# Optimization experiments

Measured on AMD Instinct MI355X. Metric: run time of the kernel, lower is better.

The kernel has to match this reference:

```python
import jax, jax.numpy as jnp
import numpy as np

# Static config (matches init_kwargs); spatial shapes must be static for jit.
SPATIAL = [(96, 96), (48, 48), (24, 24), (12, 12)]  # (H_l, W_l)
D, NH, NL, NP = 256, 8, 4, 4
DH = D // NH
DFFN = 1024


def _ln(x, g, b):
    m = jnp.mean(x, -1, keepdims=True)
    v = jnp.var(x, -1, keepdims=True)
    return (x - m) * jax.lax.rsqrt(v + 1e-5) * g + b


def _bilinear_sample(v, loc, H, W):
    # v: (N, H*W, D) projected value for one level; loc: (N,Lq,NH,NP,2) in [0,1]
    # Matches grid_sample(align_corners=False, padding_mode='zeros'):
    # pixel coord = loc * size - 0.5, zero outside.
    N = v.shape[0]
    v = v.reshape(N, H, W, NH, DH)
    x = loc[..., 0] * W - 0.5
    y = loc[..., 1] * H - 0.5
    x0 = jnp.floor(x)
    y0 = jnp.floor(y)
    wx = x - x0
    wy = y - y0
    x0i = x0.astype(jnp.int32)
    y0i = y0.astype(jnp.int32)
    b = jnp.arange(N)[:, None, None, None]
    h = jnp.arange(NH)[None, None, :, None]

    def gather(yi, xi):
        valid = (yi >= 0) & (yi < H) & (xi >= 0) & (xi < W)
        s = v[b, jnp.clip(yi, 0, H - 1), jnp.clip(xi, 0, W - 1), h]  # (N,Lq,NH,NP,DH)
        return s * valid[..., None]

    s00 = gather(y0i, x0i)
    s01 = gather(y0i, x0i + 1)
    s10 = gather(y0i + 1, x0i)
    s11 = gather(y0i + 1, x0i + 1)
    return (s00 * ((1 - wy) * (1 - wx))[..., None]
            + s01 * ((1 - wy) * wx)[..., None]
            + s10 * (wy * (1 - wx))[..., None]
            + s11 * (wy * wx)[..., None])  # (N,Lq,NH,NP,DH)


def setup_inputs() -> dict:
    key = jax.random.key(0)
    ks = jax.random.split(key, 16)
    N, Lq = 8, 1024

    def nrm(k, shp, scale=1.0):
        return jax.random.normal(k, shp, dtype=jnp.float32) * scale

    return dict(
        tgt=nrm(ks[0], (N, Lq, D)),
        reference_points=jax.random.uniform(ks[1], (N, Lq, NL, 2), dtype=jnp.float32),
        src0=nrm(ks[2], (N, 96 * 96, 16)),
        src1=nrm(ks[3], (N, 48 * 48, 32)),
        src2=nrm(ks[4], (N, 24 * 24, 16)),
        src3=nrm(ks[5], (N, 12 * 12, 32)),
        Wv0=nrm(ks[6], (16, D), 0.25), bv0=jnp.zeros((D,), jnp.float32),
        Wv1=nrm(ks[7], (32, D), 0.18), bv1=jnp.zeros((D,), jnp.float32),
        Woff=nrm(ks[8], (D, NH * NL * NP * 2), 0.01), boff=nrm(ks[9], (NH * NL * NP * 2,), 0.5),
        Wattn=nrm(ks[10], (D, NH * NL * NP), 0.01), battn=jnp.zeros((NH * NL * NP,), jnp.float32),
        Wout=nrm(ks[11], (D, D), 1.0 / 16), bout=jnp.zeros((D,), jnp.float32),
        g1=jnp.ones((D,), jnp.float32), be1=jnp.zeros((D,), jnp.float32),
        W1=nrm(ks[12], (D, DFFN), 1.0 / 16), b1=jnp.zeros((DFFN,), jnp.float32),
        W2=nrm(ks[13], (DFFN, D), 1.0 / 32), b2=jnp.zeros((D,), jnp.float32),
        g3=jnp.ones((D,), jnp.float32), be3=jnp.zeros((D,), jnp.float32),
    )


def reference(tgt, reference_points, src0, src1, src2, src3,
              Wv0, bv0, Wv1, bv1, Woff, boff, Wattn, battn, Wout, bout,
              g1, be1, W1, b1, W2, b2, g3, be3):
    N, Lq, _ = tgt.shape
    # Per-level value projection (value_{idx % (n_levels//2)}: 16->D, 32->D cycling)
    values = [src0 @ Wv0 + bv0, src1 @ Wv1 + bv1, src2 @ Wv0 + bv0, src3 @ Wv1 + bv1]

    off = (tgt @ Woff + boff).reshape(N, Lq, NH, NL, NP, 2)
    attn = jax.nn.softmax((tgt @ Wattn + battn).reshape(N, Lq, NH, NL * NP), axis=-1)
    attn = attn.reshape(N, Lq, NH, NL, NP)

    # offset_normalizer = [W_l, H_l]
    norm = jnp.array([[w, h] for (h, w) in SPATIAL], dtype=tgt.dtype)  # (NL,2)
    loc = reference_points[:, :, None, :, None, :] + off / norm[None, None, None, :, None, :]

    sampled = jnp.stack(
        [_bilinear_sample(values[l], loc[:, :, :, l], SPATIAL[l][0], SPATIAL[l][1])
         for l in range(NL)], axis=3)  # (N,Lq,NH,NL,NP,DH)
    ms_out = jnp.sum(sampled * attn[..., None], axis=(3, 4)).reshape(N, Lq, D)
    ms_out = ms_out @ Wout + bout

    # decoder layer: residual + LN, FFN + residual + LN (dropout=0 / eval)
    t = _ln(tgt + ms_out, g1, be1)
    ff = jax.nn.relu(t @ W1 + b1) @ W2 + b2
    return _ln(t + ff, g3, be3)
```

## Files before the change

### kernel.cpp

```cpp
#include <hip/hip_runtime.h>
#include <math.h>


typedef __bf16 bf16x8 __attribute__((ext_vector_type(8)));
typedef float  f32x4  __attribute__((ext_vector_type(4)));

#define VB0 0
#define VB1 18874368
#define VB2 23592960
#define VB3 24772608
#define VTOT 25067520

__device__ __forceinline__ unsigned short f2bf(float f) {
    unsigned u = __float_as_uint(f);
    u += 0x7FFF + ((u >> 16) & 1);
    return (unsigned short)(u >> 16);
}

__device__ __forceinline__ void gload16(const void* g, void* l) {
    __builtin_amdgcn_global_load_lds(
        (const __attribute__((address_space(1))) unsigned int*)g,
        (__attribute__((address_space(3))) unsigned int*)l, 16, 0, 0);
}

__global__ __launch_bounds__(256) void prep_kernel(
    const float* __restrict__ tgt, const float* __restrict__ Woff,
    const float* __restrict__ Wattn, const float* __restrict__ Wout,
    const float* __restrict__ W1, const float* __restrict__ W2,
    const float* __restrict__ boff, const float* __restrict__ battn,
    unsigned short* __restrict__ tgt_bf, unsigned short* __restrict__ Btoa,
    unsigned short* __restrict__ WoT, unsigned short* __restrict__ W1T,
    unsigned short* __restrict__ W2T, float* __restrict__ boa)
{
    __shared__ float sT[64][65];
    const int b = blockIdx.x, t = threadIdx.x;
    if (b < 2048) {
        const int i = (b * 256 + t) * 4;
        const float4 v = *(const float4*)&tgt[i];
        ushort4 o;
        o.x = f2bf(v.x); o.y = f2bf(v.y); o.z = f2bf(v.z); o.w = f2bf(v.w);
        *(ushort4*)&tgt_bf[i] = o;
        return;
    }
    if (b == 2048) {
        if (t < 384) boa[t] = (t < 256) ? boff[t] : battn[t - 256];
        return;
    }
    int tb = b - 2049;
    const float* src; unsigned short* dst; int srcN, dstK, tn, tk;
    if (tb < 16)       { src = Woff;  dst = Btoa;          srcN = 256;  dstK = 256;  tn = tb >> 2; tk = tb & 3; }
    else if (tb < 24)  { tb -= 16; src = Wattn; dst = Btoa + 65536; srcN = 128; dstK = 256; tn = tb >> 2; tk = tb & 3; }
    else if (tb < 40)  { tb -= 24; src = Wout;  dst = WoT; srcN = 256;  dstK = 256;  tn = tb >> 2; tk = tb & 3; }
    else if (tb < 104) { tb -= 40; src = W1;    dst = W1T; srcN = 1024; dstK = 256;  tn = tb >> 2; tk = tb & 3; }
    else               { tb -= 104; src = W2;   dst = W2T; srcN = 256;  dstK = 1024; tn = tb >> 4; tk = tb & 15; }
    const int n0 = tn * 64, k0 = tk * 64;
    const int j = t & 63, i0 = t >> 6;
#pragma unroll
    for (int s = 0; s < 16; ++s) {
        const int i = i0 + s * 4;
        sT[i][j] = src[(size_t)(k0 + i) * srcN + n0 + j];
    }
    __syncthreads();
#pragma unroll
    for (int s = 0; s < 16; ++s) {
        const int nr = i0 + s * 4;
        dst[(size_t)(n0 + nr) * dstK + k0 + j] = f2bf(sT[j][nr]);
    }
}

__global__ __launch_bounds__(256) void vproj_kernel(
    const float* __restrict__ src0, const float* __restrict__ src1,
    const float* __restrict__ src2, const float* __restrict__ src3,
    const float* __restrict__ Wv0, const float* __restrict__ bv0,
    const float* __restrict__ Wv1, const float* __restrict__ bv1,
    unsigned short* __restrict__ vals)
{
    __shared__ float sW[32 * 268];
    __shared__ float sS[64 * 33];

    const int b = blockIdx.x, t = threadIdx.x;
    const float *src, *W, *bias;
    int K, lb; size_t obase;
    if (b < 1152)      { src = src0; W = Wv0; bias = bv0; K = 16; lb = b;        obase = VB0; }
    else if (b < 1440) { src = src1; W = Wv1; bias = bv1; K = 32; lb = b - 1152; obase = VB1; }
    else if (b < 1512) { src = src2; W = Wv0; bias = bv0; K = 16; lb = b - 1440; obase = VB2; }
    else               { src = src3; W = Wv1; bias = bv1; K = 32; lb = b - 1512; obase = VB3; }
    const int pix0 = lb * 64;
    const int SS = K + 1;
    const int kmask = K - 1;
    const int ksh = (K == 16) ? 4 : 5;

    for (int i = t; i < K * 256; i += 256) {
        const int k = i >> 8, c = i & 255;
        sW[k * 268 + c + 4 * (c >> 6)] = W[i];
    }
    for (int i = t; i < 64 * K; i += 256) {
        sS[(i >> ksh) * SS + (i & kmask)] = src[(size_t)pix0 * K + i];
    }
    __syncthreads();

    const int p = t >> 2, cg = t & 3, cb = cg * 64;
    const int wb = cg * 68;

    float acc[64];
    {
        const float4* bp = (const float4*)&bias[cb];
#pragma unroll
        for (int j4 = 0; j4 < 16; ++j4) {
            const float4 bb = bp[j4];
            acc[j4 * 4 + 0] = bb.x; acc[j4 * 4 + 1] = bb.y;
            acc[j4 * 4 + 2] = bb.z; acc[j4 * 4 + 3] = bb.w;
        }
    }
#pragma unroll 4
    for (int k = 0; k < K; ++k) {
        const float ak = sS[p * SS + k];
        const float4* wr = (const float4*)&sW[k * 268 + wb];
#pragma unroll
        for (int j4 = 0; j4 < 16; ++j4) {
            const float4 w = wr[j4];
            acc[j4 * 4 + 0] = fmaf(ak, w.x, acc[j4 * 4 + 0]);
            acc[j4 * 4 + 1] = fmaf(ak, w.y, acc[j4 * 4 + 1]);
            acc[j4 * 4 + 2] = fmaf(ak, w.z, acc[j4 * 4 + 2]);
            acc[j4 * 4 + 3] = fmaf(ak, w.w, acc[j4 * 4 + 3]);
        }
    }
    unsigned short* op = vals + obase + (size_t)(pix0 + p) * 256 + cb;
#pragma unroll
    for (int j4 = 0; j4 < 16; ++j4) {
        ushort4 o;
        o.x = f2bf(acc[j4 * 4 + 0]); o.y = f2bf(acc[j4 * 4 + 1]);
        o.z = f2bf(acc[j4 * 4 + 2]); o.w = f2bf(acc[j4 * 4 + 3]);
        *(ushort4*)&op[j4 * 4] = o;
    }
}

template <int RELU, int OUTBF16>
__global__ __launch_bounds__(256) void gemm_bf16(
    const unsigned short* __restrict__ A, const unsigned short* __restrict__ Bt,
    const float* __restrict__ bias, float* __restrict__ C32,
    unsigned short* __restrict__ C16, int M, int N, int K)
{
    __shared__ unsigned short As[2][128 * 32];
    __shared__ unsigned short Bs[2][128 * 32];

    const int t = threadIdx.x, wv = t >> 6, l = t & 63;
    const int m0 = blockIdx.y * 128, n0 = blockIdx.x * 128;
    const int wm = wv >> 1, wn = wv & 1;
    const int lr = l >> 2, sl = l & 3;
    const int swsl = sl ^ ((lr >> 1) & 3);
    const int fr = l & 15, kg = l >> 4;
    const int rsw = (fr >> 1) & 3;

    f32x4 acc[4][4];
#pragma unroll
    for (int i = 0; i < 4; ++i)
#pragma unroll
        for (int j = 0; j < 4; ++j) acc[i][j] = (f32x4){0.f, 0.f, 0.f, 0.f};

#define STAGE(bufi, k0)                                                        \
    do {                                                                       \
        _Pragma("unroll")                                                      \
        for (int cc = 0; cc < 2; ++cc) {                                       \
            const int rb = wv * 32 + cc * 16;                                  \
            gload16(A + (size_t)(m0 + rb + lr) * K + (k0) + swsl * 8,          \
                    &As[bufi][rb * 32]);                                       \
            gload16(Bt + (size_t)(n0 + rb + lr) * K + (k0) + swsl * 8,         \
                    &Bs[bufi][rb * 32]);                                       \
        }                                                                      \
    } while (0)

    const int NT = K >> 5;
    STAGE(0, 0);
    asm volatile("s_waitcnt vmcnt(0)" ::: "memory");
    __syncthreads();

    for (int tt = 0; tt < NT; ++tt) {
        const int cur = tt & 1;
        if (tt + 1 < NT) STAGE(cur ^ 1, (tt + 1) * 32);

        bf16x8 af[4], bfr[4];
#pragma unroll
        for (int i = 0; i < 4; ++i)
            af[i] = *(const bf16x8*)&As[cur][(wm * 64 + i * 16 + fr) * 32 + (kg ^ rsw) * 8];
#pragma unroll
        for (int j = 0; j < 4; ++j)
            bfr[j] = *(const bf16x8*)&Bs[cur][(wn * 64 + j * 16 + fr) * 32 + (kg ^ rsw) * 8];
#pragma unroll
        for (int i = 0; i < 4; ++i)
#pragma unroll
            for (int j = 0; j < 4; ++j)
                acc[i][j] = __builtin_amdgcn_mfma_f32_16x16x32_bf16(af[i], bfr[j], acc[i][j], 0, 0, 0);

        asm volatile("s_waitcnt vmcnt(0)" ::: "memory");
        __syncthreads();
    }
#undef STAGE

    const int q4 = (l >> 4) * 4;
#pragma unroll
    for (int j = 0; j < 4; ++j) {
        const int col = n0 + wn * 64 + j * 16 + fr;
        const float bj = bias[col];
#pragma unroll
        for (int i = 0; i < 4; ++i) {
#pragma unroll
            for (int r = 0; r < 4; ++r) {
                const int row = m0 + wm * 64 + i * 16 + q4 + r;
                float v = acc[i][j][r] + bj;
                if (RELU) v = fmaxf(v, 0.f);
                if (OUTBF16) C16[(size_t)row * N + col] = f2bf(v);
                else         C32[(size_t)row * N + col] = v;
            }
        }
    }
}

__device__ __forceinline__ void acc8(const unsigned short* p, float w, float* a)
{
    const uint4 u = *(const uint4*)p;
    a[0] = fmaf(w, __uint_as_float(u.x << 16), a[0]);
    a[1] = fmaf(w, __uint_as_float(u.x & 0xffff0000u), a[1]);
    a[2] = fmaf(w, __uint_as_float(u.y << 16), a[2]);
    a[3] = fmaf(w, __uint_as_float(u.y & 0xffff0000u), a[3]);
    a[4] = fmaf(w, __uint_as_float(u.z << 16), a[4]);
    a[5] = fmaf(w, __uint_as_float(u.z & 0xffff0000u), a[5]);
    a[6] = fmaf(w, __uint_as_float(u.w << 16), a[6]);
    a[7] = fmaf(w, __uint_as_float(u.w & 0xffff0000u), a[7]);
}

__global__ __launch_bounds__(256) void sampler_kernel(
    const unsigned short* __restrict__ vals, const float* __restrict__ offlog,
    const float* __restrict__ ref, unsigned short* __restrict__ msout)
{
    __shared__ float sOff[8][256];
    __shared__ float sLog[8][128];
    __shared__ float sRef[8][8];

    const int t = threadIdx.x, w = t >> 6, l = t & 63;
    const int qbase = blockIdx.x * 8;

    for (int j = l; j < 768; j += 64) {
        const int second = (j >= 384);
        const int lq = w * 2 + second;
        const int jj = second ? j - 384 : j;
        const float v = offlog[(size_t)(qbase + lq) * 384 + jj];
        if (jj < 256) {
            const int h = jj >> 5, r = jj & 31;
            sOff[lq][(r >> 1) * 16 + h * 2 + (r & 1)] = v;
        } else {
            const int j2 = jj - 256;
            sLog[lq][(j2 & 15) * 8 + (j2 >> 4)] = v;
        }
    }
    if (l < 16)
        sRef[w * 2 + (l >> 3)][l & 7] = ref[(size_t)(qbase + w * 2 + (l >> 3)) * 8 + (l & 7)];
    __syncthreads();

    const int lq = w * 2 + (l >> 5);
    const int b  = qbase + lq;
    const int n  = b >> 10;
    const int h  = (l >> 2) & 7;
    const int lg = l & 3;

    float mx = -1e30f;
#pragma unroll
    for (int i = 0; i < 16; ++i) mx = fmaxf(mx, sLog[lq][i * 8 + h]);
    float e[16], s = 0.f;
#pragma unroll
    for (int i = 0; i < 16; ++i) { e[i] = __expf(sLog[lq][i * 8 + h] - mx); s += e[i]; }
    const float inv = 1.f / s;

    float acc[8] = {0.f, 0.f, 0.f, 0.f, 0.f, 0.f, 0.f, 0.f};
    const int dims[4] = {96, 48, 24, 12};
    const int hwsz[4] = {9216, 2304, 576, 144};
    const size_t vbase[4] = {VB0, VB1, VB2, VB3};

#pragma unroll
    for (int lv = 0; lv < 4; ++lv) {
        const int W = dims[lv];
        const float fx = sRef[lq][lv * 2]     * (float)W - 0.5f;
        const float fy = sRef[lq][lv * 2 + 1] * (float)W - 0.5f;
        const unsigned short* vb =
            vals + vbase[lv] + (size_t)n * hwsz[lv] * 256 + h * 32 + lg * 8;
#pragma unroll
        for (int p = 0; p < 4; ++p) {
            const float2 xy = *(const float2*)&sOff[lq][((lv * 4 + p) * 8 + h) * 2];
            const float x = fx + xy.x;
            const float y = fy + xy.y;
            const float x0f = floorf(x), y0f = floorf(y);
            const float wx = x - x0f, wy = y - y0f;
            const int x0 = (int)x0f, y0 = (int)y0f;
            const float aw = e[lv * 4 + p] * inv;
            const float vx0 = ((unsigned)x0       < (unsigned)W) ? 1.f - wx : 0.f;
            const float vx1 = ((unsigned)(x0 + 1) < (unsigned)W) ? wx       : 0.f;
            const float vy0 = ((unsigned)y0       < (unsigned)W) ? 1.f - wy : 0.f;
            const float vy1 = ((unsigned)(y0 + 1) < (unsigned)W) ? wy       : 0.f;
            const int cx0 = min(max(x0, 0), W - 1);
            const int cx1 = min(max(x0 + 1, 0), W - 1);
            const int cy0 = min(max(y0, 0), W - 1) * W;
            const int cy1 = min(max(y0 + 1, 0), W - 1) * W;
            acc8(vb + (size_t)(cy0 + cx0) * 256, aw * vy0 * vx0, acc);
            acc8(vb + (size_t)(cy0 + cx1) * 256, aw * vy0 * vx1, acc);
            acc8(vb + (size_t)(cy1 + cx0) * 256, aw * vy1 * vx0, acc);
            acc8(vb + (size_t)(cy1 + cx1) * 256, aw * vy1 * vx1, acc);
        }
    }
    uint4 o;
    o.x = (unsigned)f2bf(acc[0]) | ((unsigned)f2bf(acc[1]) << 16);
    o.y = (unsigned)f2bf(acc[2]) | ((unsigned)f2bf(acc[3]) << 16);
    o.z = (unsigned)f2bf(acc[4]) | ((unsigned)f2bf(acc[5]) << 16);
    o.w = (unsigned)f2bf(acc[6]) | ((unsigned)f2bf(acc[7]) << 16);
    *(uint4*)&msout[(size_t)b * 256 + h * 32 + lg * 8] = o;
}

__global__ __launch_bounds__(256) void ln_kernel(
    const float* __restrict__ a, const float* __restrict__ b,
    const float* __restrict__ g, const float* __restrict__ be,
    float* __restrict__ out32, unsigned short* __restrict__ out16)
{
    const int t = threadIdx.x, w = t >> 6, l = t & 63;
    const int row = blockIdx.x * 4 + w;
    const size_t base = (size_t)row * 256 + l * 4;
    const float4 av = *(const float4*)&a[base];
    const float4 bv = *(const float4*)&b[base];
    const float x0 = av.x + bv.x, x1 = av.y + bv.y, x2 = av.z + bv.z, x3 = av.w + bv.w;
    float s  = x0 + x1 + x2 + x3;
    float s2 = x0 * x0 + x1 * x1 + x2 * x2 + x3 * x3;
#pragma unroll
    for (int o = 32; o; o >>= 1) { s += __shfl_xor(s, o); s2 += __shfl_xor(s2, o); }
    const float mean = s * (1.f / 256.f);
    const float rstd = rsqrtf(s2 * (1.f / 256.f) - mean * mean + 1e-5f);
    const float4 gv = *(const float4*)&g[l * 4];
    const float4 ev = *(const float4*)&be[l * 4];
    const float y0 = (x0 - mean) * rstd * gv.x + ev.x;
    const float y1 = (x1 - mean) * rstd * gv.y + ev.y;
    const float y2 = (x2 - mean) * rstd * gv.z + ev.z;
    const float y3 = (x3 - mean) * rstd * gv.w + ev.w;
    float4 o4; o4.x = y0; o4.y = y1; o4.z = y2; o4.w = y3;
    *(float4*)&out32[base] = o4;
    if (out16) {
        ushort4 o;
        o.x = f2bf(y0); o.y = f2bf(y1); o.z = f2bf(y2); o.w = f2bf(y3);
        *(ushort4*)&out16[base] = o;
    }
}

extern "C" void kernel_launch(void* const* d_in, const int* in_sizes, int n_in,
                              void* d_out, int out_size, void* d_ws, size_t ws_size,
                              hipStream_t stream)
{
    const float* tgt   = (const float*)d_in[0];
    const float* ref   = (const float*)d_in[1];
    const float* src0  = (const float*)d_in[2];
    const float* src1  = (const float*)d_in[3];
    const float* src2  = (const float*)d_in[4];
    const float* src3  = (const float*)d_in[5];
    const float* Wv0   = (const float*)d_in[6];
    const float* bv0   = (const float*)d_in[7];
    const float* Wv1   = (const float*)d_in[8];
    const float* bv1   = (const float*)d_in[9];
    const float* Woff  = (const float*)d_in[10];
    const float* boff  = (const float*)d_in[11];
    const float* Wattn = (const float*)d_in[12];
    const float* battn = (const float*)d_in[13];
    const float* Wout  = (const float*)d_in[14];
    const float* bout  = (const float*)d_in[15];
    const float* g1    = (const float*)d_in[16];
    const float* be1   = (const float*)d_in[17];
    const float* W1    = (const float*)d_in[18];
    const float* b1    = (const float*)d_in[19];
    const float* W2    = (const float*)d_in[20];
    const float* b2    = (const float*)d_in[21];
    const float* g3    = (const float*)d_in[22];
    const float* be3   = (const float*)d_in[23];

    char* w8 = (char*)d_ws;
    unsigned short* vals_bf  = (unsigned short*)(w8 + 0);
    unsigned short* tgt_bf   = (unsigned short*)(w8 + 50135040);
    unsigned short* Btoa     = (unsigned short*)(w8 + 54329344);
    unsigned short* WoT      = (unsigned short*)(w8 + 54525952);
    unsigned short* W1T      = (unsigned short*)(w8 + 54657024);
    unsigned short* W2T      = (unsigned short*)(w8 + 55181312);
    unsigned short* ffn1_bf  = (unsigned short*)(w8 + 55705600);
    unsigned short* msout_bf = (unsigned short*)(w8 + 72482816);
    unsigned short* tbuf16   = (unsigned short*)(w8 + 76677120);
    float* boa    = (float*)(w8 + 80871424);
    float* offlog = (float*)(w8 + 80872960);
    float* ms2    = (float*)(w8 + 93455872);
    float* tbuf32 = (float*)(w8 + 101844480);
    float* ffn2   = (float*)(w8 + 110233088);

    const dim3 blk(256);

    prep_kernel<<<2217, blk, 0, stream>>>(tgt, Woff, Wattn, Wout, W1, W2, boff, battn,
                                          tgt_bf, Btoa, WoT, W1T, W2T, boa);
    vproj_kernel<<<1530, blk, 0, stream>>>(src0, src1, src2, src3, Wv0, bv0, Wv1, bv1, vals_bf);

    gemm_bf16<0, 0><<<dim3(3, 64), blk, 0, stream>>>(tgt_bf, Btoa, boa, offlog,
                                                     (unsigned short*)nullptr, 8192, 384, 256);
    sampler_kernel<<<1024, blk, 0, stream>>>(vals_bf, offlog, ref, msout_bf);

    gemm_bf16<0, 0><<<dim3(2, 64), blk, 0, stream>>>(msout_bf, WoT, bout, ms2,
                                                     (unsigned short*)nullptr, 8192, 256, 256);
    ln_kernel<<<2048, blk, 0, stream>>>(tgt, ms2, g1, be1, tbuf32, tbuf16);

    gemm_bf16<1, 1><<<dim3(8, 64), blk, 0, stream>>>(tbuf16, W1T, b1, (float*)nullptr,
                                                     ffn1_bf, 8192, 1024, 256);
    gemm_bf16<0, 0><<<dim3(2, 64), blk, 0, stream>>>(ffn1_bf, W2T, b2, ffn2,
                                                     (unsigned short*)nullptr, 8192, 256, 1024);
    ln_kernel<<<2048, blk, 0, stream>>>(tbuf32, ffn2, g3, be3, (float*)d_out,
                                        (unsigned short*)nullptr);
}
```

Before: 234.7 us.

## Replace FP32 value projection kernel with bf16 MFMA GEMMs over padded sources

```diff
diff --git a/kernel.cpp b/kernel.cpp
--- a/kernel.cpp
+++ b/kernel.cpp
@@ -28,9 +28,15 @@
     const float* __restrict__ Wattn, const float* __restrict__ Wout,
     const float* __restrict__ W1, const float* __restrict__ W2,
     const float* __restrict__ boff, const float* __restrict__ battn,
+    const float* __restrict__ src0, const float* __restrict__ src1,
+    const float* __restrict__ src2, const float* __restrict__ src3,
+    const float* __restrict__ Wv0, const float* __restrict__ Wv1,
     unsigned short* __restrict__ tgt_bf, unsigned short* __restrict__ Btoa,
     unsigned short* __restrict__ WoT, unsigned short* __restrict__ W1T,
-    unsigned short* __restrict__ W2T, float* __restrict__ boa)
+    unsigned short* __restrict__ W2T, float* __restrict__ boa,
+    unsigned short* __restrict__ src0p, unsigned short* __restrict__ src1b,
+    unsigned short* __restrict__ src2p, unsigned short* __restrict__ src3b,
+    unsigned short* __restrict__ WvT0, unsigned short* __restrict__ WvT1)
 {
     __shared__ float sT[64][65];
     const int b = blockIdx.x, t = threadIdx.x;
@@ -44,6 +50,46 @@
     }
     if (b == 2048) {
         if (t < 384) boa[t] = (t < 256) ? boff[t] : battn[t - 256];
+#pragma unroll
+        for (int k = 0; k < 16; ++k) {
+            WvT0[t * 32 + k]      = f2bf(Wv0[k * 256 + t]);
+            WvT0[t * 32 + 16 + k] = 0;
+        }
+#pragma unroll
+        for (int k = 0; k < 32; ++k)
+            WvT1[t * 32 + k] = f2bf(Wv1[k * 256 + t]);
+        return;
+    }
+    if (b >= 2217) {
+        const int q = (b - 2217) * 256 + t;
+        if (q < 294912) {
+            const float4 v = *(const float4*)&src0[(size_t)q * 4];
+            ushort4 o;
+            o.x = f2bf(v.x); o.y = f2bf(v.y); o.z = f2bf(v.z); o.w = f2bf(v.w);
+            const int px = q >> 2, qt = q & 3;
+            *(ushort4*)&src0p[(size_t)px * 32 + qt * 4] = o;
+            *(ushort4*)&src0p[(size_t)px * 32 + 16 + qt * 4] = (ushort4){0, 0, 0, 0};
+        } else if (q < 442368) {
+            const int q2 = q - 294912;
+            const float4 v = *(const float4*)&src1[(size_t)q2 * 4];
+            ushort4 o;
+            o.x = f2bf(v.x); o.y = f2bf(v.y); o.z = f2bf(v.z); o.w = f2bf(v.w);
+            *(ushort4*)&src1b[(size_t)q2 * 4] = o;
+        } else if (q < 460800) {
+            const int q3 = q - 442368;
+            const float4 v = *(const float4*)&src2[(size_t)q3 * 4];
+            ushort4 o;
+            o.x = f2bf(v.x); o.y = f2bf(v.y); o.z = f2bf(v.z); o.w = f2bf(v.w);
+            const int px = q3 >> 2, qt = q3 & 3;
+            *(ushort4*)&src2p[(size_t)px * 32 + qt * 4] = o;
+            *(ushort4*)&src2p[(size_t)px * 32 + 16 + qt * 4] = (ushort4){0, 0, 0, 0};
+        } else if (q < 470016) {
+            const int q4 = q - 460800;
+            const float4 v = *(const float4*)&src3[(size_t)q4 * 4];
+            ushort4 o;
+            o.x = f2bf(v.x); o.y = f2bf(v.y); o.z = f2bf(v.z); o.w = f2bf(v.w);
+            *(ushort4*)&src3b[(size_t)q4 * 4] = o;
+        }
         return;
     }
     int tb = b - 2049;
@@ -65,73 +111,6 @@
     for (int s = 0; s < 16; ++s) {
         const int nr = i0 + s * 4;
         dst[(size_t)(n0 + nr) * dstK + k0 + j] = f2bf(sT[j][nr]);
-    }
-}
-
-__global__ __launch_bounds__(256) void vproj_kernel(
-    const float* __restrict__ src0, const float* __restrict__ src1,
-    const float* __restrict__ src2, const float* __restrict__ src3,
-    const float* __restrict__ Wv0, const float* __restrict__ bv0,
-    const float* __restrict__ Wv1, const float* __restrict__ bv1,
-    unsigned short* __restrict__ vals)
-{
-    __shared__ float sW[32 * 268];
-    __shared__ float sS[64 * 33];
-
-    const int b = blockIdx.x, t = threadIdx.x;
-    const float *src, *W, *bias;
-    int K, lb; size_t obase;
-    if (b < 1152)      { src = src0; W = Wv0; bias = bv0; K = 16; lb = b;        obase = VB0; }
-    else if (b < 1440) { src = src1; W = Wv1; bias = bv1; K = 32; lb = b - 1152; obase = VB1; }
-    else if (b < 1512) { src = src2; W = Wv0; bias = bv0; K = 16; lb = b - 1440; obase = VB2; }
-    else               { src = src3; W = Wv1; bias = bv1; K = 32; lb = b - 1512; obase = VB3; }
-    const int pix0 = lb * 64;
-    const int SS = K + 1;
-    const int kmask = K - 1;
-    const int ksh = (K == 16) ? 4 : 5;
-
-    for (int i = t; i < K * 256; i += 256) {
-        const int k = i >> 8, c = i & 255;
-        sW[k * 268 + c + 4 * (c >> 6)] = W[i];
-    }
-    for (int i = t; i < 64 * K; i += 256) {
-        sS[(i >> ksh) * SS + (i & kmask)] = src[(size_t)pix0 * K + i];
-    }
-    __syncthreads();
-
-    const int p = t >> 2, cg = t & 3, cb = cg * 64;
-    const int wb = cg * 68;
-
-    float acc[64];
-    {
-        const float4* bp = (const float4*)&bias[cb];
-#pragma unroll
-        for (int j4 = 0; j4 < 16; ++j4) {
-            const float4 bb = bp[j4];
-            acc[j4 * 4 + 0] = bb.x; acc[j4 * 4 + 1] = bb.y;
-            acc[j4 * 4 + 2] = bb.z; acc[j4 * 4 + 3] = bb.w;
-        }
-    }
-#pragma unroll 4
-    for (int k = 0; k < K; ++k) {
-        const float ak = sS[p * SS + k];
-        const float4* wr = (const float4*)&sW[k * 268 + wb];
-#pragma unroll
-        for (int j4 = 0; j4 < 16; ++j4) {
-            const float4 w = wr[j4];
-            acc[j4 * 4 + 0] = fmaf(ak, w.x, acc[j4 * 4 + 0]);
-            acc[j4 * 4 + 1] = fmaf(ak, w.y, acc[j4 * 4 + 1]);
-            acc[j4 * 4 + 2] = fmaf(ak, w.z, acc[j4 * 4 + 2]);
-            acc[j4 * 4 + 3] = fmaf(ak, w.w, acc[j4 * 4 + 3]);
-        }
-    }
-    unsigned short* op = vals + obase + (size_t)(pix0 + p) * 256 + cb;
-#pragma unroll
-    for (int j4 = 0; j4 < 16; ++j4) {
-        ushort4 o;
-        o.x = f2bf(acc[j4 * 4 + 0]); o.y = f2bf(acc[j4 * 4 + 1]);
-        o.z = f2bf(acc[j4 * 4 + 2]); o.w = f2bf(acc[j4 * 4 + 3]);
-        *(ushort4*)&op[j4 * 4] = o;
     }
 }
 
@@ -390,12 +369,28 @@
     float* ms2    = (float*)(w8 + 93455872);
     float* tbuf32 = (float*)(w8 + 101844480);
     float* ffn2   = (float*)(w8 + 110233088);
+    unsigned short* src0p = (unsigned short*)(w8 + 93455872);
+    unsigned short* src1b = (unsigned short*)(w8 + 93455872 + 4718592);
+    unsigned short* src2p = (unsigned short*)(w8 + 93455872 + 5898240);
+    unsigned short* src3b = (unsigned short*)(w8 + 93455872 + 6193152);
+    unsigned short* WvT0  = (unsigned short*)(w8 + 93455872 + 6266880);
+    unsigned short* WvT1  = (unsigned short*)(w8 + 93455872 + 6283264);
 
     const dim3 blk(256);
 
-    prep_kernel<<<2217, blk, 0, stream>>>(tgt, Woff, Wattn, Wout, W1, W2, boff, battn,
-                                          tgt_bf, Btoa, WoT, W1T, W2T, boa);
-    vproj_kernel<<<1530, blk, 0, stream>>>(src0, src1, src2, src3, Wv0, bv0, Wv1, bv1, vals_bf);
+    prep_kernel<<<4053, blk, 0, stream>>>(tgt, Woff, Wattn, Wout, W1, W2, boff, battn,
+                                          src0, src1, src2, src3, Wv0, Wv1,
+                                          tgt_bf, Btoa, WoT, W1T, W2T, boa,
+                                          src0p, src1b, src2p, src3b, WvT0, WvT1);
+
+    gemm_bf16<0, 1><<<dim3(2, 576), blk, 0, stream>>>(src0p, WvT0, bv0, (float*)nullptr,
+                                                      vals_bf + VB0, 73728, 256, 32);
+    gemm_bf16<0, 1><<<dim3(2, 144), blk, 0, stream>>>(src1b, WvT1, bv1, (float*)nullptr,
+                                                      vals_bf + VB1, 18432, 256, 32);
+    gemm_bf16<0, 1><<<dim3(2, 36),  blk, 0, stream>>>(src2p, WvT0, bv0, (float*)nullptr,
+                                                      vals_bf + VB2, 4608, 256, 32);
+    gemm_bf16<0, 1><<<dim3(2, 9),   blk, 0, stream>>>(src3b, WvT1, bv1, (float*)nullptr,
+                                                      vals_bf + VB3, 1152, 256, 32);
 
     gemm_bf16<0, 0><<<dim3(3, 64), blk, 0, stream>>>(tgt_bf, Btoa, boa, offlog,
                                                      (unsigned short*)nullptr, 8192, 384, 256);
```

Result: faster. 222.9 us (-5.0%).
